# Kernel optimization log

Hardware: AMD Instinct MI355X
Metric: run time of the kernel (lower is better)

The kernel has to match this reference:

```python
import jax, jax.numpy as jnp
import numpy as np
from jax import lax

B, W, L, E, V, C, H, O = 16384, 5, 20, 50, 100000, 128, 4096, 50


def setup_inputs() -> dict:
    key = jax.random.key(0)
    ks = jax.random.split(key, 10)
    x = jax.random.randint(ks[0], (B, W), 1, V)
    word_id_to_chars_ids = jax.random.randint(ks[1], (V, L), 0, C)
    word_emb = jax.random.normal(ks[2], (V, E), dtype=jnp.float32) * 0.1
    word_emb = word_emb.at[0].set(0.0)  # padding_idx=0
    char_emb = jax.random.normal(ks[3], (C, E), dtype=jnp.float32) * 0.1
    char_emb = char_emb.at[0].set(0.0)  # padding_idx=0
    conv_w = jax.random.normal(ks[4], (E, E, 3), dtype=jnp.float32) * (1.0 / np.sqrt(E * 3))
    conv_b = jax.random.normal(ks[5], (E,), dtype=jnp.float32) * 0.01
    fc1_w = jax.random.normal(ks[6], (H, E * W), dtype=jnp.float32) * (1.0 / np.sqrt(E * W))
    fc1_b = jnp.zeros((H,), dtype=jnp.float32)
    fc2_w = jax.random.normal(ks[7], (O, H), dtype=jnp.float32) * (1.0 / np.sqrt(H))
    fc2_b = jnp.zeros((O,), dtype=jnp.float32)
    return {"x": x, "word_id_to_chars_ids": word_id_to_chars_ids,
            "word_emb": word_emb, "char_emb": char_emb,
            "conv_w": conv_w, "conv_b": conv_b,
            "fc1_w": fc1_w, "fc1_b": fc1_b, "fc2_w": fc2_w, "fc2_b": fc2_b}


def reference(x, word_id_to_chars_ids, word_emb, char_emb, conv_w, conv_b,
              fc1_w, fc1_b, fc2_w, fc2_b):
    # per-window char ids: [B, 5, L] -> char embeddings [B, 5, L, E]
    char_ids = word_id_to_chars_ids[x]
    ce = char_emb[char_ids]
    # conv1d over char positions: reshape to NCW = [B*5, E, L]
    ce = ce.reshape(B * W, L, E).transpose(0, 2, 1)
    conv = lax.conv_general_dilated(ce, conv_w, window_strides=(1,),
                                    padding=[(1, 1)],
                                    dimension_numbers=("NCH", "OIH", "NCH"))
    conv = conv + conv_b[None, :, None]
    # max-pool over char positions (kernel == L): [B*5, E] -> [B, 5, E]
    chars = jnp.max(conv, axis=2).reshape(B, W, E)
    words = word_emb[x]  # [B, 5, E]
    h = (words + chars).reshape(B, W * E)  # view(-1, 250)
    h = jnp.tanh(h @ fc1_w.T + fc1_b)
    logits = h @ fc2_w.T + fc2_b
    return jax.nn.softmax(logits, axis=1)
```

## Files before the change

### kernel.cpp

```cpp
#include <hip/hip_runtime.h>
#include <hip/hip_bf16.h>


typedef __attribute__((ext_vector_type(8))) short short8;
typedef __attribute__((ext_vector_type(4))) float float4v;

__device__ inline short bf16b(float f) {
    __hip_bfloat16 h = __float2bfloat16(f);
    return *reinterpret_cast<short*>(&h);
}
__device__ inline uint packbf2(float a, float b) {
    return (uint)(ushort)bf16b(a) | ((uint)(ushort)bf16b(b) << 16);
}
__device__ inline void gload_lds16(const void* g, void* l) {
    __builtin_amdgcn_global_load_lds(
        (const __attribute__((address_space(1))) unsigned int*)g,
        (__attribute__((address_space(3))) unsigned int*)l, 16, 0, 0);
}

__global__ void wbf_kernel(const float* __restrict__ fc1_w,
                           const float* __restrict__ fc1_b,
                           short* __restrict__ wbf) {
    int idx = blockIdx.x * 256 + threadIdx.x;
    int n = idx >> 8, k = idx & 255;
    float v = (k < 250) ? fc1_w[n * 250 + k] : (k == 250 ? fc1_b[n] : 0.f);
    int CT = n >> 4, mm = n & 15;
    int ks = k >> 5, qq = (k >> 3) & 3, j = k & 7;
    wbf[((CT * 8 + ks) * 64 + qq * 16 + mm) * 8 + j] = bf16b(v);
}

__global__ void w2bf_kernel(const float* __restrict__ fc2_w,
                            short* __restrict__ w2bf) {
    int idx = blockIdx.x * 256 + threadIdx.x;
    int o = idx >> 12, k = idx & 4095;
    float v = (o < 50) ? fc2_w[idx] : 0.f;
    int Ot = o >> 4, mm = o & 15;
    int kst = k >> 5, qq = (k >> 3) & 3, j = k & 7;
    w2bf[((kst * 4 + Ot) * 64 + qq * 16 + mm) * 8 + j] = bf16b(v);
}

__global__ void gt_kernel(const float* __restrict__ char_emb,
                          const float* __restrict__ conv_w,
                          float* __restrict__ gt) {
    int idx = blockIdx.x * 256 + threadIdx.x;
    if (idx >= 19200) return;
    int c = idx / 150, rem = idx - c * 150;
    int kk = rem / 50, o = rem - kk * 50;
    const float* ce = char_emb + c * 50;
    const float* w  = conv_w + o * 150 + kk;
    float s = 0.f;
    #pragma unroll 10
    for (int i = 0; i < 50; ++i) s += ce[i] * w[i * 3];
    gt[c * 156 + kk * 52 + o] = s;
}

__global__ void haPad_kernel(__hip_bfloat16* __restrict__ ha) {
    int idx = blockIdx.x * 256 + threadIdx.x;
    int b = idx / 6, j = idx - b * 6;
    ha[b * 256 + 250 + j] = __float2bfloat16(j == 0 ? 1.f : 0.f);
}

__global__ __launch_bounds__(512) void conv_kernel(
    const int* __restrict__ x, const int* __restrict__ wci,
    const float* __restrict__ word_emb, const float* __restrict__ conv_b,
    const float* __restrict__ gt, __hip_bfloat16* __restrict__ ha)
{
    __shared__ float Gs[19968];
    __shared__ uint  cpack[160];
    __shared__ int   xs[32];

    const int tid = threadIdx.x;
    const int gw0 = blockIdx.x * 32;

    int xr = 0;
    if (tid < 32) xr = x[gw0 + tid];

    #pragma unroll
    for (int t = 0; t < 39; ++t)
        Gs[t * 512 + tid] = gt[t * 512 + tid];

    if (tid < 32) {
        const int* crow = wci + xr * 20;
        int cid[20];
        #pragma unroll
        for (int p = 0; p < 20; ++p) cid[p] = crow[p];
        #pragma unroll
        for (int u = 0; u < 5; ++u)
            cpack[tid * 5 + u] = (uint)cid[u * 4] | ((uint)cid[u * 4 + 1] << 8)
                               | ((uint)cid[u * 4 + 2] << 16) | ((uint)cid[u * 4 + 3] << 24);
        xs[tid] = xr;
    }
    __syncthreads();

    const int lane = tid & 63;
    const int wv   = tid >> 6;
    const int t    = lane & 15;
    const int w    = lane >> 4;
    const int tc   = (t < 13) ? t : 12;
    const int widx = wv * 4 + w;

    uint cw[5];
    #pragma unroll
    for (int u = 0; u < 5; ++u) cw[u] = cpack[widx * 5 + u];
    int ca[20];
    #pragma unroll
    for (int p = 0; p < 20; ++p)
        ca[p] = (int)((cw[p >> 2] >> ((p & 3) * 8)) & 0xFF) * 156;

    const int tc4 = tc * 4;
    float4 mx;
    {
        float4 v = *(const float4*)&Gs[ca[0] + 52 + tc4];
        float4 u = *(const float4*)&Gs[ca[1] + 104 + tc4];
        mx.x = v.x + u.x; mx.y = v.y + u.y; mx.z = v.z + u.z; mx.w = v.w + u.w;
    }
    #pragma unroll
    for (int l = 1; l < 19; ++l) {
        float4 v = *(const float4*)&Gs[ca[l] + 52 + tc4];
        float4 a = *(const float4*)&Gs[ca[l - 1] + tc4];
        float4 b = *(const float4*)&Gs[ca[l + 1] + 104 + tc4];
        float vx = v.x + a.x + b.x, vy = v.y + a.y + b.y;
        float vz = v.z + a.z + b.z, vw = v.w + a.w + b.w;
        mx.x = fmaxf(mx.x, vx); mx.y = fmaxf(mx.y, vy);
        mx.z = fmaxf(mx.z, vz); mx.w = fmaxf(mx.w, vw);
    }
    {
        float4 v = *(const float4*)&Gs[ca[19] + 52 + tc4];
        float4 a = *(const float4*)&Gs[ca[18] + tc4];
        mx.x = fmaxf(mx.x, v.x + a.x); mx.y = fmaxf(mx.y, v.y + a.y);
        mx.z = fmaxf(mx.z, v.z + a.z); mx.w = fmaxf(mx.w, v.w + a.w);
    }

    const int xid = xs[widx];
    const float* wer = word_emb + (size_t)xid * 50 + tc4;
    float2 wea = *(const float2*)wer;
    float2 web = make_float2(0.f, 0.f);
    float2 cba = *(const float2*)(conv_b + tc4);
    float2 cbb = make_float2(0.f, 0.f);
    if (tc < 12) {
        web = *(const float2*)(wer + 2);
        cbb = *(const float2*)(conv_b + tc4 + 2);
    }
    const int gw = gw0 + widx, b = gw / 5, wp = gw - b * 5;
    __hip_bfloat16* dst = ha + b * 256 + wp * 50 + tc4;
    uint lo = packbf2(mx.x + cba.x + wea.x, mx.y + cba.y + wea.y);
    if (t < 12) {
        uint hi = packbf2(mx.z + cbb.x + web.x, mx.w + cbb.y + web.y);
        *(uint*)dst = lo;
        *((uint*)dst + 1) = hi;
    } else if (t == 12) {
        *(uint*)dst = lo;
    }
}

__global__ __launch_bounds__(512, 1) void fused_kernel(
    const __hip_bfloat16* __restrict__ ha, const short* __restrict__ wbf,
    const short* __restrict__ w2bf, const float* __restrict__ fc2_b,
    float* __restrict__ out)
{
    __shared__ char smem[147456];
    short8* Bsv = (short8*)smem;
    char*   hsb = smem + 131072;
    float*  partf = (float*)smem;

    const int tid  = threadIdx.x;
    const int lane = tid & 63;
    const int wv   = tid >> 6;
    const int wm = wv >> 2, wn = wv & 3;
    const int q = lane >> 4, m = lane & 15;
    const int m0 = blockIdx.x * 64;
    const int wt = wv * 64;

    const short8* wbfv  = (const short8*)wbf;
    const short8* w2bfv = (const short8*)w2bf;
    const short8* hav   = (const short8*)ha;

    short8 av[2][8];
    #pragma unroll
    for (int mt = 0; mt < 2; ++mt)
        #pragma unroll
        for (int ks = 0; ks < 8; ++ks)
            av[mt][ks] = hav[(size_t)(m0 + wm * 32 + mt * 16 + m) * 32 + ks * 4 + q];
    #pragma unroll
    for (int mt = 0; mt < 2; ++mt)
        #pragma unroll
        for (int ks = 0; ks < 8; ++ks)
            asm volatile("" : "+v"(av[mt][ks]));

    #pragma unroll
    for (int i = 0; i < 8; ++i)
        gload_lds16(wbfv + i * 512 + tid, Bsv + i * 512 + wt);
    __syncthreads();

    float4v acc2[4][2] = {};

    for (int ch = 0; ch < 32; ++ch) {
        const int buf = ch & 1;

        short8 b2[2];
        #pragma unroll
        for (int Otp = 0; Otp < 2; ++Otp)
            b2[Otp] = w2bfv[(size_t)((ch * 4 + wn) * 4 + wm * 2 + Otp) * 64 + lane];

        if (ch < 31) {
            #pragma unroll
            for (int i = 0; i < 8; ++i)
                gload_lds16(wbfv + (size_t)(ch + 1) * 4096 + i * 512 + tid,
                            Bsv + (buf ^ 1) * 4096 + i * 512 + wt);
        }

        float4v acc[2][2] = {};
        #pragma unroll
        for (int ks = 0; ks < 8; ++ks) {
            short8 bv[2];
            #pragma unroll
            for (int nt = 0; nt < 2; ++nt)
                bv[nt] = Bsv[buf * 4096 + ((wn * 2 + nt) * 8 + ks) * 64 + lane];
            #pragma unroll
            for (int mt = 0; mt < 2; ++mt)
                #pragma unroll
                for (int nt = 0; nt < 2; ++nt)
                    acc[mt][nt] = __builtin_amdgcn_mfma_f32_16x16x32_bf16(
                        bv[nt], av[mt][ks], acc[mt][nt], 0, 0, 0);
        }

        const int q2base = q >> 1, slot = q & 1;
        #pragma unroll
        for (int mt = 0; mt < 2; ++mt) {
            const int Rl = wm * 2 + mt;
            #pragma unroll
            for (int nt = 0; nt < 2; ++nt) {
                float tv[4];
                #pragma unroll
                for (int r = 0; r < 4; ++r)
                    tv[r] = 1.f - 2.f / (__expf(2.f * acc[mt][nt][r]) + 1.f);
                const int q2 = nt * 2 + q2base;
                const uint p0 = packbf2(tv[0], tv[1]);
                const uint p1 = packbf2(tv[2], tv[3]);
                *(uint2*)(hsb + (((Rl * 4 + wn) * 64 + q2 * 16 + m) * 16 + slot * 8))
                    = make_uint2(p0, p1);
            }
        }

        asm volatile("s_waitcnt lgkmcnt(0)" ::: "memory");
        __builtin_amdgcn_sched_barrier(0);
        __builtin_amdgcn_s_barrier();

        {
            short8 a2[4];
            #pragma unroll
            for (int Rl = 0; Rl < 4; ++Rl)
                a2[Rl] = *(const short8*)(hsb + ((Rl * 4 + wn) * 64 + lane) * 16);
            #pragma unroll
            for (int Rl = 0; Rl < 4; ++Rl)
                #pragma unroll
                for (int Otp = 0; Otp < 2; ++Otp)
                    acc2[Rl][Otp] = __builtin_amdgcn_mfma_f32_16x16x32_bf16(
                        a2[Rl], b2[Otp], acc2[Rl][Otp], 0, 0, 0);
        }

        __syncthreads();
    }

    #pragma unroll
    for (int Rl = 0; Rl < 4; ++Rl)
        #pragma unroll
        for (int Otp = 0; Otp < 2; ++Otp)
            #pragma unroll
            for (int r = 0; r < 4; ++r)
                partf[(wn * 64 + Rl * 16 + q * 4 + r) * 64
                      + wm * 32 + Otp * 16 + m] = acc2[Rl][Otp][r];
    __syncthreads();

    #pragma unroll
    for (int t = 0; t < 8; ++t) {
        int idx = t * 512 + tid;
        int row = idx >> 6, col = idx & 63;
        float lg = partf[row * 64 + col] + partf[(64 + row) * 64 + col]
                 + partf[(128 + row) * 64 + col] + partf[(192 + row) * 64 + col];
        partf[row * 64 + col] = (col < 50) ? lg + fc2_b[col] : -1e30f;
    }
    __syncthreads();

    #pragma unroll
    for (int rr = 0; rr < 8; ++rr) {
        const int row = wv * 8 + rr;
        float v = partf[row * 64 + lane];
        float mx = v;
        #pragma unroll
        for (int off = 32; off > 0; off >>= 1) mx = fmaxf(mx, __shfl_xor(mx, off));
        float e = __expf(v - mx);
        float s = e;
        #pragma unroll
        for (int off = 32; off > 0; off >>= 1) s += __shfl_xor(s, off);
        if (lane < 50)
            out[(size_t)(m0 + row) * 50 + lane] = e / s;
    }
}

extern "C" void kernel_launch(void* const* d_in, const int* in_sizes, int n_in,
                              void* d_out, int out_size, void* d_ws, size_t ws_size,
                              hipStream_t stream) {
    const int*   x        = (const int*)  d_in[0];
    const int*   wci      = (const int*)  d_in[1];
    const float* word_emb = (const float*)d_in[2];
    const float* char_emb = (const float*)d_in[3];
    const float* conv_w   = (const float*)d_in[4];
    const float* conv_b   = (const float*)d_in[5];
    const float* fc1_w    = (const float*)d_in[6];
    const float* fc1_b    = (const float*)d_in[7];
    const float* fc2_w    = (const float*)d_in[8];
    const float* fc2_b    = (const float*)d_in[9];
    float* out = (float*)d_out;

    char* ws = (char*)d_ws;
    __hip_bfloat16* ha  = (__hip_bfloat16*)ws;
    short* wbf  = (short*)(ws + ((size_t)8  << 20));
    short* w2bf = (short*)(ws + ((size_t)10 << 20));
    float* gtp  = (float*)(ws + ((size_t)11 << 20));

    wbf_kernel<<<4096, 256, 0, stream>>>(fc1_w, fc1_b, wbf);
    w2bf_kernel<<<1024, 256, 0, stream>>>(fc2_w, w2bf);
    gt_kernel<<<75, 256, 0, stream>>>(char_emb, conv_w, gtp);
    haPad_kernel<<<384, 256, 0, stream>>>(ha);
    conv_kernel<<<2560, 512, 0, stream>>>(x, wci, word_emb, conv_b, gtp, ha);
    fused_kernel<<<256, 512, 0, stream>>>(ha, wbf, w2bf, fc2_b, out);
}
```

Measured before the change: 211.0 us.

## Split fused MLP over hidden dimension across two blocks and merge prep kernels

Merges the four small preprocessing kernels into one launch to cut launch overhead. The fused fc1/tanh/fc2 kernel is split so each block handles half of the hidden chunks for 64 rows, doubling the grid to 512 blocks and halving LDS to allow two blocks per CU. Partial logits are written to a workspace buffer and a new combine kernel sums them, adds the bias and applies softmax. In exchange it drops double-buffering of the weight tiles (the next tile is loaded after the barrier), raises MFMA priority, and adds an extra kernel plus a global round-trip for the partial logits.

```diff
diff --git a/kernel.cpp b/kernel.cpp
--- a/kernel.cpp
+++ b/kernel.cpp
@@ -18,46 +18,44 @@
         (__attribute__((address_space(3))) unsigned int*)l, 16, 0, 0);
 }
 
-__global__ void wbf_kernel(const float* __restrict__ fc1_w,
-                           const float* __restrict__ fc1_b,
-                           short* __restrict__ wbf) {
-    int idx = blockIdx.x * 256 + threadIdx.x;
-    int n = idx >> 8, k = idx & 255;
-    float v = (k < 250) ? fc1_w[n * 250 + k] : (k == 250 ? fc1_b[n] : 0.f);
-    int CT = n >> 4, mm = n & 15;
-    int ks = k >> 5, qq = (k >> 3) & 3, j = k & 7;
-    wbf[((CT * 8 + ks) * 64 + qq * 16 + mm) * 8 + j] = bf16b(v);
-}
-
-__global__ void w2bf_kernel(const float* __restrict__ fc2_w,
-                            short* __restrict__ w2bf) {
-    int idx = blockIdx.x * 256 + threadIdx.x;
-    int o = idx >> 12, k = idx & 4095;
-    float v = (o < 50) ? fc2_w[idx] : 0.f;
-    int Ot = o >> 4, mm = o & 15;
-    int kst = k >> 5, qq = (k >> 3) & 3, j = k & 7;
-    w2bf[((kst * 4 + Ot) * 64 + qq * 16 + mm) * 8 + j] = bf16b(v);
-}
-
-__global__ void gt_kernel(const float* __restrict__ char_emb,
-                          const float* __restrict__ conv_w,
-                          float* __restrict__ gt) {
-    int idx = blockIdx.x * 256 + threadIdx.x;
-    if (idx >= 19200) return;
-    int c = idx / 150, rem = idx - c * 150;
-    int kk = rem / 50, o = rem - kk * 50;
-    const float* ce = char_emb + c * 50;
-    const float* w  = conv_w + o * 150 + kk;
-    float s = 0.f;
-    #pragma unroll 10
-    for (int i = 0; i < 50; ++i) s += ce[i] * w[i * 3];
-    gt[c * 156 + kk * 52 + o] = s;
-}
-
-__global__ void haPad_kernel(__hip_bfloat16* __restrict__ ha) {
-    int idx = blockIdx.x * 256 + threadIdx.x;
-    int b = idx / 6, j = idx - b * 6;
-    ha[b * 256 + 250 + j] = __float2bfloat16(j == 0 ? 1.f : 0.f);
+__global__ __launch_bounds__(256) void prep_kernel(
+    const float* __restrict__ fc1_w, const float* __restrict__ fc1_b,
+    const float* __restrict__ fc2_w, const float* __restrict__ char_emb,
+    const float* __restrict__ conv_w, short* __restrict__ wbf,
+    short* __restrict__ w2bf, float* __restrict__ gt,
+    __hip_bfloat16* __restrict__ ha)
+{
+    const int bid = blockIdx.x;
+    if (bid < 4096) {
+        int idx = bid * 256 + threadIdx.x;
+        int n = idx >> 8, k = idx & 255;
+        float v = (k < 250) ? fc1_w[n * 250 + k] : (k == 250 ? fc1_b[n] : 0.f);
+        int CT = n >> 4, mm = n & 15;
+        int ks = k >> 5, qq = (k >> 3) & 3, j = k & 7;
+        wbf[((CT * 8 + ks) * 64 + qq * 16 + mm) * 8 + j] = bf16b(v);
+    } else if (bid < 5120) {
+        int idx = (bid - 4096) * 256 + threadIdx.x;
+        int o = idx >> 12, k = idx & 4095;
+        float v = (o < 50) ? fc2_w[idx] : 0.f;
+        int Ot = o >> 4, mm = o & 15;
+        int kst = k >> 5, qq = (k >> 3) & 3, j = k & 7;
+        w2bf[((kst * 4 + Ot) * 64 + qq * 16 + mm) * 8 + j] = bf16b(v);
+    } else if (bid < 5195) {
+        int idx = (bid - 5120) * 256 + threadIdx.x;
+        if (idx >= 19200) return;
+        int c = idx / 150, rem = idx - c * 150;
+        int kk = rem / 50, o = rem - kk * 50;
+        const float* ce = char_emb + c * 50;
+        const float* w  = conv_w + o * 150 + kk;
+        float s = 0.f;
+        #pragma unroll 10
+        for (int i = 0; i < 50; ++i) s += ce[i] * w[i * 3];
+        gt[c * 156 + kk * 52 + o] = s;
+    } else {
+        int idx = (bid - 5195) * 256 + threadIdx.x;
+        int b = idx / 6, j = idx - b * 6;
+        ha[b * 256 + 250 + j] = __float2bfloat16(j == 0 ? 1.f : 0.f);
+    }
 }
 
 __global__ __launch_bounds__(512) void conv_kernel(
@@ -153,110 +151,104 @@
     }
 }
 
-__global__ __launch_bounds__(512, 1) void fused_kernel(
+__global__ __launch_bounds__(512, 2) void fused_kernel(
     const __hip_bfloat16* __restrict__ ha, const short* __restrict__ wbf,
-    const short* __restrict__ w2bf, const float* __restrict__ fc2_b,
-    float* __restrict__ out)
+    const short* __restrict__ w2bf, float* __restrict__ gpart)
 {
-    __shared__ char smem[147456];
+    __shared__ char smem[81920];
     short8* Bsv = (short8*)smem;
-    char*   hsb = smem + 131072;
+    char*   hsb = smem + 65536;
     float*  partf = (float*)smem;
 
     const int tid  = threadIdx.x;
     const int lane = tid & 63;
     const int wv   = tid >> 6;
-    const int wm = wv >> 2, wn = wv & 3;
+    const int wr = wv >> 1, wc = wv & 1;
     const int q = lane >> 4, m = lane & 15;
-    const int m0 = blockIdx.x * 64;
-    const int wt = wv * 64;
+    const int rg = blockIdx.x >> 1, kh = blockIdx.x & 1;
+    const int m0 = rg * 64;
+    const int ch0 = kh * 16;
 
     const short8* wbfv  = (const short8*)wbf;
     const short8* w2bfv = (const short8*)w2bf;
     const short8* hav   = (const short8*)ha;
 
-    short8 av[2][8];
-    #pragma unroll
-    for (int mt = 0; mt < 2; ++mt)
-        #pragma unroll
-        for (int ks = 0; ks < 8; ++ks)
-            av[mt][ks] = hav[(size_t)(m0 + wm * 32 + mt * 16 + m) * 32 + ks * 4 + q];
-    #pragma unroll
-    for (int mt = 0; mt < 2; ++mt)
-        #pragma unroll
-        for (int ks = 0; ks < 8; ++ks)
-            asm volatile("" : "+v"(av[mt][ks]));
+    short8 av[8];
+    #pragma unroll
+    for (int ks = 0; ks < 8; ++ks)
+        av[ks] = hav[(size_t)(m0 + wr * 16 + m) * 32 + ks * 4 + q];
+    #pragma unroll
+    for (int ks = 0; ks < 8; ++ks)
+        asm volatile("" : "+v"(av[ks]));
 
     #pragma unroll
     for (int i = 0; i < 8; ++i)
-        gload_lds16(wbfv + i * 512 + tid, Bsv + i * 512 + wt);
+        gload_lds16(wbfv + (size_t)ch0 * 4096 + i * 512 + tid,
+                    Bsv + i * 512 + tid);
     __syncthreads();
 
     float4v acc2[4][2] = {};
 
-    for (int ch = 0; ch < 32; ++ch) {
-        const int buf = ch & 1;
+    for (int chl = 0; chl < 16; ++chl) {
+        const int ch = ch0 + chl;
 
         short8 b2[2];
         #pragma unroll
         for (int Otp = 0; Otp < 2; ++Otp)
-            b2[Otp] = w2bfv[(size_t)((ch * 4 + wn) * 4 + wm * 2 + Otp) * 64 + lane];
-
-        if (ch < 31) {
-            #pragma unroll
-            for (int i = 0; i < 8; ++i)
-                gload_lds16(wbfv + (size_t)(ch + 1) * 4096 + i * 512 + tid,
-                            Bsv + (buf ^ 1) * 4096 + i * 512 + wt);
+            b2[Otp] = w2bfv[(size_t)((ch * 4 + wr) * 4 + wc * 2 + Otp) * 64 + lane];
+
+        float4v acc[4] = {};
+        #pragma unroll
+        for (int ks = 0; ks < 8; ++ks) {
+            short8 bv[4];
+            #pragma unroll
+            for (int nt = 0; nt < 4; ++nt)
+                bv[nt] = Bsv[((wc * 4 + nt) * 8 + ks) * 64 + lane];
+            #pragma unroll
+            for (int nt = 0; nt < 4; ++nt)
+                acc[nt] = __builtin_amdgcn_mfma_f32_16x16x32_bf16(
+                    bv[nt], av[ks], acc[nt], 0, 0, 0);
         }
 
-        float4v acc[2][2] = {};
-        #pragma unroll
-        for (int ks = 0; ks < 8; ++ks) {
-            short8 bv[2];
-            #pragma unroll
-            for (int nt = 0; nt < 2; ++nt)
-                bv[nt] = Bsv[buf * 4096 + ((wn * 2 + nt) * 8 + ks) * 64 + lane];
-            #pragma unroll
-            for (int mt = 0; mt < 2; ++mt)
-                #pragma unroll
-                for (int nt = 0; nt < 2; ++nt)
-                    acc[mt][nt] = __builtin_amdgcn_mfma_f32_16x16x32_bf16(
-                        bv[nt], av[mt][ks], acc[mt][nt], 0, 0, 0);
-        }
-
         const int q2base = q >> 1, slot = q & 1;
         #pragma unroll
-        for (int mt = 0; mt < 2; ++mt) {
-            const int Rl = wm * 2 + mt;
-            #pragma unroll
-            for (int nt = 0; nt < 2; ++nt) {
-                float tv[4];
-                #pragma unroll
-                for (int r = 0; r < 4; ++r)
-                    tv[r] = 1.f - 2.f / (__expf(2.f * acc[mt][nt][r]) + 1.f);
-                const int q2 = nt * 2 + q2base;
-                const uint p0 = packbf2(tv[0], tv[1]);
-                const uint p1 = packbf2(tv[2], tv[3]);
-                *(uint2*)(hsb + (((Rl * 4 + wn) * 64 + q2 * 16 + m) * 16 + slot * 8))
-                    = make_uint2(p0, p1);
-            }
+        for (int nt = 0; nt < 4; ++nt) {
+            float tv[4];
+            #pragma unroll
+            for (int r = 0; r < 4; ++r)
+                tv[r] = 1.f - 2.f / (__expf(2.f * acc[nt][r]) + 1.f);
+            const int ks2l = wc * 2 + (nt >> 1);
+            const int q2 = (nt & 1) * 2 + q2base;
+            const uint p0 = packbf2(tv[0], tv[1]);
+            const uint p1 = packbf2(tv[2], tv[3]);
+            *(uint2*)(hsb + (((wr * 4 + ks2l) * 64 + q2 * 16 + m) * 16 + slot * 8))
+                = make_uint2(p0, p1);
         }
 
         asm volatile("s_waitcnt lgkmcnt(0)" ::: "memory");
         __builtin_amdgcn_sched_barrier(0);
         __builtin_amdgcn_s_barrier();
 
+        if (chl < 15) {
+            #pragma unroll
+            for (int i = 0; i < 8; ++i)
+                gload_lds16(wbfv + (size_t)(ch + 1) * 4096 + i * 512 + tid,
+                            Bsv + i * 512 + tid);
+        }
+
         {
             short8 a2[4];
             #pragma unroll
             for (int Rl = 0; Rl < 4; ++Rl)
-                a2[Rl] = *(const short8*)(hsb + ((Rl * 4 + wn) * 64 + lane) * 16);
+                a2[Rl] = *(const short8*)(hsb + ((Rl * 4 + wr) * 64 + lane) * 16);
+            __builtin_amdgcn_s_setprio(1);
             #pragma unroll
             for (int Rl = 0; Rl < 4; ++Rl)
                 #pragma unroll
                 for (int Otp = 0; Otp < 2; ++Otp)
                     acc2[Rl][Otp] = __builtin_amdgcn_mfma_f32_16x16x32_bf16(
                         a2[Rl], b2[Otp], acc2[Rl][Otp], 0, 0, 0);
+            __builtin_amdgcn_s_setprio(0);
         }
 
         __syncthreads();
@@ -268,24 +260,35 @@
         for (int Otp = 0; Otp < 2; ++Otp)
             #pragma unroll
             for (int r = 0; r < 4; ++r)
-                partf[(wn * 64 + Rl * 16 + q * 4 + r) * 64
-                      + wm * 32 + Otp * 16 + m] = acc2[Rl][Otp][r];
+                partf[(size_t)wr * 4096 + (Rl * 16 + q * 4 + r) * 64
+                      + wc * 32 + Otp * 16 + m] = acc2[Rl][Otp][r];
     __syncthreads();
 
     #pragma unroll
     for (int t = 0; t < 8; ++t) {
         int idx = t * 512 + tid;
-        int row = idx >> 6, col = idx & 63;
-        float lg = partf[row * 64 + col] + partf[(64 + row) * 64 + col]
-                 + partf[(128 + row) * 64 + col] + partf[(192 + row) * 64 + col];
-        partf[row * 64 + col] = (col < 50) ? lg + fc2_b[col] : -1e30f;
-    }
-    __syncthreads();
+        float s = partf[idx] + partf[4096 + idx]
+                + partf[8192 + idx] + partf[12288 + idx];
+        gpart[(size_t)blockIdx.x * 4096 + idx] = s;
+    }
+}
+
+__global__ __launch_bounds__(256) void combine_kernel(
+    const float* __restrict__ gpart, const float* __restrict__ fc2_b,
+    float* __restrict__ out)
+{
+    const int tid  = threadIdx.x;
+    const int lane = tid & 63;
+    const int wv   = tid >> 6;
+    const float bias = (lane < 50) ? fc2_b[lane] : 0.f;
 
     #pragma unroll
     for (int rr = 0; rr < 8; ++rr) {
-        const int row = wv * 8 + rr;
-        float v = partf[row * 64 + lane];
+        const int row = blockIdx.x * 32 + wv * 8 + rr;
+        const int rg = row >> 6, rl = row & 63;
+        float v = gpart[(size_t)(rg * 2) * 4096 + rl * 64 + lane]
+                + gpart[(size_t)(rg * 2 + 1) * 4096 + rl * 64 + lane];
+        v = (lane < 50) ? v + bias : -1e30f;
         float mx = v;
         #pragma unroll
         for (int off = 32; off > 0; off >>= 1) mx = fmaxf(mx, __shfl_xor(mx, off));
@@ -294,7 +297,7 @@
         #pragma unroll
         for (int off = 32; off > 0; off >>= 1) s += __shfl_xor(s, off);
         if (lane < 50)
-            out[(size_t)(m0 + row) * 50 + lane] = e / s;
+            out[(size_t)row * 50 + lane] = e / s;
     }
 }
 
@@ -315,14 +318,14 @@
 
     char* ws = (char*)d_ws;
     __hip_bfloat16* ha  = (__hip_bfloat16*)ws;
-    short* wbf  = (short*)(ws + ((size_t)8  << 20));
-    short* w2bf = (short*)(ws + ((size_t)10 << 20));
-    float* gtp  = (float*)(ws + ((size_t)11 << 20));
-
-    wbf_kernel<<<4096, 256, 0, stream>>>(fc1_w, fc1_b, wbf);
-    w2bf_kernel<<<1024, 256, 0, stream>>>(fc2_w, w2bf);
-    gt_kernel<<<75, 256, 0, stream>>>(char_emb, conv_w, gtp);
-    haPad_kernel<<<384, 256, 0, stream>>>(ha);
+    short* wbf   = (short*)(ws + ((size_t)8  << 20));
+    short* w2bf  = (short*)(ws + ((size_t)10 << 20));
+    float* gtp   = (float*)(ws + ((size_t)11 << 20));
+    float* gpart = (float*)(ws + ((size_t)16 << 20));
+
+    prep_kernel<<<5579, 256, 0, stream>>>(fc1_w, fc1_b, fc2_w, char_emb,
+                                          conv_w, wbf, w2bf, gtp, ha);
     conv_kernel<<<2560, 512, 0, stream>>>(x, wci, word_emb, conv_b, gtp, ha);
-    fused_kernel<<<256, 512, 0, stream>>>(ha, wbf, w2bf, fc2_b, out);
-}
+    fused_kernel<<<512, 512, 0, stream>>>(ha, wbf, w2bf, gpart);
+    combine_kernel<<<512, 256, 0, stream>>>(gpart, fc2_b, out);
+}
```

Result: slower. 223.5 us (+5.9%).
